# Optimization experiments

Measured on AMD Instinct MI355X. Metric: run time of the kernel, lower is better.

## Reference

```python
import jax, jax.numpy as jnp
import numpy as np

NUM_HEADS = 12

def setup_inputs() -> dict:
    key = jax.random.key(0)
    k1, k2, k3 = jax.random.split(key, 3)
    B, N, D = 16, 1024, 768
    x = jax.random.normal(k1, (B, N, D), dtype=jnp.float32)
    w_qkv = jax.random.normal(k2, (D, 3 * D), dtype=jnp.float32) * (D ** -0.5)
    b_qkv = jnp.zeros((3 * D,), dtype=jnp.float32)
    w_proj = jax.random.normal(k3, (D, D), dtype=jnp.float32) * (D ** -0.5)
    b_proj = jnp.zeros((D,), dtype=jnp.float32)
    return {"x": x, "w_qkv": w_qkv, "b_qkv": b_qkv, "w_proj": w_proj, "b_proj": b_proj}

def reference(x, w_qkv, b_qkv, w_proj, b_proj):
    B, N, D = x.shape
    H = NUM_HEADS
    Hd = D // H
    scale = Hd ** -0.5
    qkv = x @ w_qkv + b_qkv                       # (B, N, 3D)
    qkv = qkv.reshape(B, N, 3, H, Hd)
    q, k, v = qkv[:, :, 0], qkv[:, :, 1], qkv[:, :, 2]  # (B, N, H, Hd)
    attn = jnp.einsum('bnhd,bmhd->bhnm', q, k) * scale  # (B, H, N, N)
    attn = jax.nn.softmax(attn, axis=-1)
    out = jnp.einsum('bhnm,bmhd->bnhd', attn, v).reshape(B, N, D)
    return out @ w_proj + b_proj
```

## Files before the change

kernel.cpp:

```cpp
#include <hip/hip_runtime.h>


typedef _Float16 half8 __attribute__((ext_vector_type(8)));
typedef _Float16 half4 __attribute__((ext_vector_type(4)));
typedef __fp16   fp16x2 __attribute__((ext_vector_type(2)));
typedef float    f32x4  __attribute__((ext_vector_type(4)));
typedef float    f32x16 __attribute__((ext_vector_type(16)));
typedef unsigned int u32x4 __attribute__((ext_vector_type(4)));

#define DI __device__ __forceinline__

constexpr int   BATCH  = 16;
constexpr int   SEQ    = 1024;
constexpr int   DM     = 768;
constexpr int   NH     = 12;
constexpr int   HD     = 64;
constexpr float SCALE  = 0.125f;
constexpr float LOG2E  = 1.4426950408889634f;

DI void copy16(_Float16* dst, const _Float16* src) {
  *(u32x4*)dst = *(const u32x4*)src;
}

DI int pack_rtz(float a, float b) {
  union { fp16x2 h; int i; } u;
  u.h = __builtin_amdgcn_cvt_pkrtz(a, b);
  return u.i;
}

__global__ void cvt_x_kernel(const float* __restrict__ x,
                             _Float16* __restrict__ xh, int n4) {
  int i = blockIdx.x * 256 + threadIdx.x;
  if (i >= n4) return;
  float4 v = ((const float4*)x)[i];
  half4 h;
  h[0] = (_Float16)v.x; h[1] = (_Float16)v.y;
  h[2] = (_Float16)v.z; h[3] = (_Float16)v.w;
  *(half4*)(xh + (size_t)i * 4) = h;
}

__global__ void cvt_wt2_kernel(const float* __restrict__ wq,
                               _Float16* __restrict__ wqT,
                               const float* __restrict__ wp,
                               _Float16* __restrict__ wpT) {
  __shared__ float tile[32][33];
  const int by = blockIdx.y;
  const float* w; _Float16* wt; int N, nb;
  if (by < 72) { w = wq; wt = wqT; N = 2304; nb = by * 32; }
  else         { w = wp; wt = wpT; N = 768;  nb = (by - 72) * 32; }
  const int K = 768;
  int kb = blockIdx.x * 32;
  int tx = threadIdx.x & 31, ty = threadIdx.x >> 5;
#pragma unroll
  for (int i = 0; i < 32; i += 8)
    tile[ty + i][tx] = w[(size_t)(kb + ty + i) * N + nb + tx];
  __syncthreads();
#pragma unroll
  for (int i = 0; i < 32; i += 8)
    wt[(size_t)(nb + ty + i) * K + kb + tx] = (_Float16)tile[tx][ty + i];
}

__launch_bounds__(256, 3)
__global__ void gemm_qkv_kernel(const _Float16* __restrict__ A,
                                const _Float16* __restrict__ Bt,
                                const float* __restrict__ bias,
                                _Float16* __restrict__ Qo,
                                _Float16* __restrict__ Ko,
                                _Float16* __restrict__ VTo) {
  __shared__ _Float16 sh[20480];
  _Float16* Cs = sh;
  const int tid  = threadIdx.x;
  const int lin  = blockIdx.x;
  const int xcd  = lin & 7, j = lin >> 3;
  const int ct   = j % 18;
  const int m0   = ((j / 18) * 8 + xcd) * 128;
  const int n0   = ct * 128;
  const int w    = tid >> 6, lane = tid & 63;
  const int quad = lane >> 4, l15 = lane & 15;
  const int wr   = w >> 1, wc = w & 1;

  f32x4 acc[4][4] = {};

  const int e  = tid * 8;
  const int rA = e >> 5;
  const int g8 = e & 31;
  const _Float16* ga = A  + (size_t)(m0 + rA) * 768 + g8;
  const _Float16* gb = Bt + (size_t)(n0 + rA) * 768 + g8;
  const int so = rA * 40 + g8;

  u32x4 pA0 = *(const u32x4*)ga;
  u32x4 pA1 = *(const u32x4*)(ga + 64 * 768);
  u32x4 pB0 = *(const u32x4*)gb;
  u32x4 pB1 = *(const u32x4*)(gb + 64 * 768);
  {
    _Float16* As = sh; _Float16* Bs = sh + 5120;
    *(u32x4*)(As + so) = pA0; *(u32x4*)(As + so + 64 * 40) = pA1;
    *(u32x4*)(Bs + so) = pB0; *(u32x4*)(Bs + so + 64 * 40) = pB1;
  }

  for (int kt = 0; kt < 24; ++kt) {
    __syncthreads();
    if (kt < 23) {
      const int k0 = (kt + 1) * 32;
      pA0 = *(const u32x4*)(ga + k0);
      pA1 = *(const u32x4*)(ga + k0 + 64 * 768);
      pB0 = *(const u32x4*)(gb + k0);
      pB1 = *(const u32x4*)(gb + k0 + 64 * 768);
    }
    const _Float16* As = sh + (kt & 1) * 10240;
    const _Float16* Bs = As + 5120;

    half8 af[4], bf[4];
#pragma unroll
    for (int mi = 0; mi < 4; mi++)
      af[mi] = *(const half8*)&As[(wr * 64 + mi * 16 + l15) * 40 + quad * 8];
#pragma unroll
    for (int ni = 0; ni < 4; ni++)
      bf[ni] = *(const half8*)&Bs[(wc * 64 + ni * 16 + l15) * 40 + quad * 8];
#pragma unroll
    for (int mi = 0; mi < 4; mi++)
#pragma unroll
      for (int ni = 0; ni < 4; ni++)
        acc[mi][ni] = __builtin_amdgcn_mfma_f32_16x16x32_f16(
            af[mi], bf[ni], acc[mi][ni], 0, 0, 0);

    if (kt < 23) {
      _Float16* Asn = sh + ((kt + 1) & 1) * 10240;
      _Float16* Bsn = Asn + 5120;
      *(u32x4*)(Asn + so) = pA0; *(u32x4*)(Asn + so + 64 * 40) = pA1;
      *(u32x4*)(Bsn + so) = pB0; *(u32x4*)(Bsn + so + 64 * 40) = pB1;
    }
  }
  __syncthreads();

  const float oscale = (ct < 6) ? SCALE : 1.0f;
  float bcol[4];
#pragma unroll
  for (int ni = 0; ni < 4; ni++)
    bcol[ni] = bias[n0 + wc * 64 + ni * 16 + l15];

  const int b     = m0 >> 10;
  const int nrow0 = m0 & 1023;
  const int sec   = ct / 6;
  const int h0    = (ct % 6) * 2;

#pragma unroll
  for (int p = 0; p < 2; ++p) {
    if (p) __syncthreads();
    if (wr == p) {
#pragma unroll
      for (int mi = 0; mi < 4; mi++)
#pragma unroll
        for (int ni = 0; ni < 4; ni++) {
          int col = wc * 64 + ni * 16 + l15;
          int row = mi * 16 + quad * 4;
#pragma unroll
          for (int r = 0; r < 4; r++)
            Cs[(row + r) * 136 + col] =
                (_Float16)((acc[mi][ni][r] + bcol[ni]) * oscale);
        }
    }
    __syncthreads();

    if (sec < 2) {
      _Float16* dst = (sec == 0) ? Qo : Ko;
      int row = tid >> 2, seg = tid & 3;
      int hl = seg >> 1, off32 = (seg & 1) * 32;
      _Float16* g = dst +
          ((size_t)((b * NH + h0 + hl) * SEQ + nrow0 + p * 64 + row)) * HD + off32;
      const _Float16* s = &Cs[row * 136 + hl * 64 + off32];
      copy16(g, s);
      copy16(g + 8, s + 8);
      copy16(g + 16, s + 16);
      copy16(g + 24, s + 24);
    } else {
      int c = tid & 127, half = tid >> 7;
      int hl = c >> 6, d = c & 63;
      _Float16 tmp[32];
#pragma unroll
      for (int jj = 0; jj < 32; jj++) tmp[jj] = Cs[(half * 32 + jj) * 136 + c];
      _Float16* g = VTo + ((size_t)((b * NH + h0 + hl) * HD + d)) * SEQ
                        + nrow0 + p * 64 + half * 32;
#pragma unroll
      for (int jj = 0; jj < 4; jj++)
        copy16(g + jj * 8, (const _Float16*)&tmp[jj * 8]);
    }
  }
}

__launch_bounds__(256, 2)
__global__ void attn_kernel(const _Float16* __restrict__ Q,
                            const _Float16* __restrict__ K,
                            const _Float16* __restrict__ VT,
                            _Float16* __restrict__ Oh) {
  __shared__ _Float16 smem[2][2][64 * 72];
  _Float16* OLds = &smem[0][0][0];

  const int tid = threadIdx.x;
  const int i   = blockIdx.x;
  const int bh  = (i & 7) * 24 + ((i >> 3) >> 2);
  const int q0  = ((i >> 3) & 3) * 256;
  const int b   = bh / NH, hh = bh - b * NH;
  const int w   = tid >> 6, lane = tid & 63;
  const int l31 = lane & 31, h = lane >> 5;

  const _Float16* Qg = Q  + (size_t)bh * SEQ * HD;
  const _Float16* Kg = K  + (size_t)bh * SEQ * HD;
  const _Float16* Vg = VT + (size_t)bh * HD * SEQ;

  half8 qb[2][4];
#pragma unroll
  for (int N = 0; N < 2; N++) {
    const _Float16* qrow = Qg + (size_t)(q0 + w * 64 + N * 32 + l31) * HD + h * 8;
#pragma unroll
    for (int s = 0; s < 4; s++)
      qb[N][s] = *(const half8*)(qrow + s * 16);
  }

  const int  sr  = (tid & 127) >> 1;
  const int  sp  = tid & 1;
  const bool isK = tid < 128;
  const _Float16* sg = isK ? (Kg + sr * HD + sp * 32)
                           : (Vg + (size_t)sr * SEQ + sp * 32);
  const int sstep = isK ? 64 * HD : 64;
  const int soff  = (isK ? 0 : 64 * 72) + sr * 72 + sp * 32;

  u32x4 pf[4];
#pragma unroll
  for (int c = 0; c < 4; c++) pf[c] = *(const u32x4*)(sg + c * 8);
#pragma unroll
  for (int c = 0; c < 4; c++) *(u32x4*)(&smem[0][0][0] + soff + c * 8) = pf[c];

  f32x16 of[2][2];
#pragma unroll
  for (int D = 0; D < 2; D++)
#pragma unroll
    for (int N = 0; N < 2; N++)
#pragma unroll
      for (int r = 0; r < 16; r++) of[D][N][r] = 0.f;
  float m_[2] = {-1e30f, -1e30f}, l_[2] = {0.f, 0.f};

  for (int kt = 0; kt < 16; ++kt) {
    if (kt < 15) {
      const _Float16* nsg = sg + (kt + 1) * sstep;
#pragma unroll
      for (int c = 0; c < 4; c++) pf[c] = *(const u32x4*)(nsg + c * 8);
    }
    __syncthreads();
    const _Float16* Ks = &smem[kt & 1][0][0];
    const _Float16* Vs = &smem[kt & 1][1][0];

    f32x16 sf[2][2];
#pragma unroll
    for (int M = 0; M < 2; M++)
#pragma unroll
      for (int N = 0; N < 2; N++)
#pragma unroll
        for (int r = 0; r < 16; r++) sf[M][N][r] = 0.f;
#pragma unroll
    for (int s = 0; s < 4; s++) {
      half8 ka0 = *(const half8*)&Ks[l31 * 72 + s * 16 + h * 8];
      half8 ka1 = *(const half8*)&Ks[(32 + l31) * 72 + s * 16 + h * 8];
#pragma unroll
      for (int N = 0; N < 2; N++) {
        sf[0][N] = __builtin_amdgcn_mfma_f32_32x32x16_f16(ka0, qb[N][s], sf[0][N], 0, 0, 0);
        sf[1][N] = __builtin_amdgcn_mfma_f32_32x32x16_f16(ka1, qb[N][s], sf[1][N], 0, 0, 0);
      }
    }

    float alpha[2], c1[2], tsum[2];
#pragma unroll
    for (int N = 0; N < 2; N++) {
      float tmax = -1e30f;
#pragma unroll
      for (int r = 0; r < 16; r++)
        tmax = fmaxf(tmax, fmaxf(sf[0][N][r], sf[1][N][r]));
      tmax = fmaxf(tmax, __shfl_xor(tmax, 32, 64));
      float mnew = fmaxf(m_[N], tmax);
      alpha[N] = __builtin_amdgcn_exp2f((m_[N] - mnew) * LOG2E);
      m_[N] = mnew;
      c1[N] = mnew * LOG2E;
      tsum[N] = 0.f;
    }

    int pdw[2][2][8];
#pragma unroll
    for (int M = 0; M < 2; M++)
#pragma unroll
      for (int N = 0; N < 2; N++) {
#pragma unroll
        for (int r = 0; r < 16; r++) {
          float p = __builtin_amdgcn_exp2f(sf[M][N][r] * LOG2E - c1[N]);
          sf[M][N][r] = p;
          tsum[N] += p;
        }
#pragma unroll
        for (int u = 0; u < 8; u++)
          pdw[M][N][u] = pack_rtz(sf[M][N][2 * u], sf[M][N][2 * u + 1]);
      }
#pragma unroll
    for (int N = 0; N < 2; N++) {
      tsum[N] += __shfl_xor(tsum[N], 32, 64);
      l_[N] = l_[N] * alpha[N] + tsum[N];
    }
#pragma unroll
    for (int D = 0; D < 2; D++)
#pragma unroll
      for (int N = 0; N < 2; N++)
#pragma unroll
        for (int r = 0; r < 16; r++) of[D][N][r] *= alpha[N];

#pragma unroll
    for (int t = 0; t < 4; ++t) {
      const int M = t >> 1, s2 = (t & 1) * 4;
      half8 va0 = *(const half8*)&Vs[l31 * 72 + t * 16 + h * 8];
      half8 va1 = *(const half8*)&Vs[(32 + l31) * 72 + t * 16 + h * 8];
#pragma unroll
      for (int N = 0; N < 2; N++) {
        int a0 = pdw[M][N][s2 + 0], a1 = pdw[M][N][s2 + 1];
        int a2 = pdw[M][N][s2 + 2], a3 = pdw[M][N][s2 + 3];
        int e0 = h ? a0 : a2, e1 = h ? a1 : a3;
        int r0 = __shfl_xor(e0, 32, 64), r1 = __shfl_xor(e1, 32, 64);
        union { u32x4 u; half8 hv; } bb;
        bb.u[0] = h ? r0 : a0; bb.u[1] = h ? r1 : a1;
        bb.u[2] = h ? a2 : r0; bb.u[3] = h ? a3 : r1;
        of[0][N] = __builtin_amdgcn_mfma_f32_32x32x16_f16(va0, bb.hv, of[0][N], 0, 0, 0);
        of[1][N] = __builtin_amdgcn_mfma_f32_32x32x16_f16(va1, bb.hv, of[1][N], 0, 0, 0);
      }
    }

    if (kt < 15) {
      _Float16* dst = &smem[(kt + 1) & 1][0][0] + soff;
#pragma unroll
      for (int c = 0; c < 4; c++) *(u32x4*)(dst + c * 8) = pf[c];
    }
  }

  __syncthreads();
  float inv[2] = {1.0f / l_[0], 1.0f / l_[1]};
  int* OW = (int*)OLds;
#pragma unroll
  for (int N = 0; N < 2; N++) {
    const int q_local = w * 64 + N * 32 + l31;
#pragma unroll
    for (int D = 0; D < 2; D++)
#pragma unroll
      for (int u = 0; u < 8; u++) {
        int v = pack_rtz(of[D][N][2 * u] * inv[N], of[D][N][2 * u + 1] * inv[N]);
        int dwi = 16 * D + 4 * (u >> 1) + (u & 1) + 2 * h;
        OW[q_local * 36 + dwi] = v;
      }
  }
  __syncthreads();
#pragma unroll
  for (int p = 0; p < 8; p++) {
    int q = p * 32 + (tid >> 3), c = tid & 7;
    *(u32x4*)(Oh + (size_t)(b * SEQ + q0 + q) * DM + hh * HD + c * 8) =
        *(const u32x4*)&OLds[q * 72 + c * 8];
  }
}

__launch_bounds__(256, 3)
__global__ void gemm_proj_kernel(const _Float16* __restrict__ A,
                                 const _Float16* __restrict__ Bt,
                                 const float* __restrict__ bias,
                                 float* __restrict__ out) {
  __shared__ _Float16 sh[20480];
  const int tid  = threadIdx.x;
  const int lin  = blockIdx.x;
  const int xcd  = lin & 7, j = lin >> 3;
  const int ct   = j % 6;
  const int m0   = ((j / 6) * 8 + xcd) * 128;
  const int n0   = ct * 128;
  const int w    = tid >> 6, lane = tid & 63;
  const int quad = lane >> 4, l15 = lane & 15;
  const int wr   = w >> 1, wc = w & 1;

  f32x4 acc[4][4] = {};

  const int e  = tid * 8;
  const int rA = e >> 5;
  const int g8 = e & 31;
  const _Float16* ga = A  + (size_t)(m0 + rA) * 768 + g8;
  const _Float16* gb = Bt + (size_t)(n0 + rA) * 768 + g8;
  const int so = rA * 40 + g8;

  u32x4 pA0 = *(const u32x4*)ga;
  u32x4 pA1 = *(const u32x4*)(ga + 64 * 768);
  u32x4 pB0 = *(const u32x4*)gb;
  u32x4 pB1 = *(const u32x4*)(gb + 64 * 768);
  {
    _Float16* As = sh; _Float16* Bs = sh + 5120;
    *(u32x4*)(As + so) = pA0; *(u32x4*)(As + so + 64 * 40) = pA1;
    *(u32x4*)(Bs + so) = pB0; *(u32x4*)(Bs + so + 64 * 40) = pB1;
  }

  for (int kt = 0; kt < 24; ++kt) {
    __syncthreads();
    if (kt < 23) {
      const int k0 = (kt + 1) * 32;
      pA0 = *(const u32x4*)(ga + k0);
      pA1 = *(const u32x4*)(ga + k0 + 64 * 768);
      pB0 = *(const u32x4*)(gb + k0);
      pB1 = *(const u32x4*)(gb + k0 + 64 * 768);
    }
    const _Float16* As = sh + (kt & 1) * 10240;
    const _Float16* Bs = As + 5120;

    half8 af[4], bf[4];
#pragma unroll
    for (int mi = 0; mi < 4; mi++)
      af[mi] = *(const half8*)&As[(wr * 64 + mi * 16 + l15) * 40 + quad * 8];
#pragma unroll
    for (int ni = 0; ni < 4; ni++)
      bf[ni] = *(const half8*)&Bs[(wc * 64 + ni * 16 + l15) * 40 + quad * 8];
#pragma unroll
    for (int mi = 0; mi < 4; mi++)
#pragma unroll
      for (int ni = 0; ni < 4; ni++)
        acc[mi][ni] = __builtin_amdgcn_mfma_f32_16x16x32_f16(
            af[mi], bf[ni], acc[mi][ni], 0, 0, 0);

    if (kt < 23) {
      _Float16* Asn = sh + ((kt + 1) & 1) * 10240;
      _Float16* Bsn = Asn + 5120;
      *(u32x4*)(Asn + so) = pA0; *(u32x4*)(Asn + so + 64 * 40) = pA1;
      *(u32x4*)(Bsn + so) = pB0; *(u32x4*)(Bsn + so + 64 * 40) = pB1;
    }
  }

  float bcol[4];
#pragma unroll
  for (int ni = 0; ni < 4; ni++)
    bcol[ni] = bias[n0 + wc * 64 + ni * 16 + l15];
#pragma unroll
  for (int mi = 0; mi < 4; mi++)
#pragma unroll
    for (int ni = 0; ni < 4; ni++) {
      int col = n0 + wc * 64 + ni * 16 + l15;
      int row = m0 + wr * 64 + mi * 16 + quad * 4;
#pragma unroll
      for (int r = 0; r < 4; r++)
        out[(size_t)(row + r) * 768 + col] = acc[mi][ni][r] + bcol[ni];
    }
}

extern "C" void kernel_launch(void* const* d_in, const int* in_sizes, int n_in,
                              void* d_out, int out_size, void* d_ws, size_t ws_size,
                              hipStream_t stream) {
  const float* x      = (const float*)d_in[0];
  const float* w_qkv  = (const float*)d_in[1];
  const float* b_qkv  = (const float*)d_in[2];
  const float* w_proj = (const float*)d_in[3];
  const float* b_proj = (const float*)d_in[4];
  float* out = (float*)d_out;

  char* ws = (char*)d_ws;
  _Float16* xh     = (_Float16*)(ws);
  _Float16* wqkvT  = (_Float16*)(ws + 25165824);
  _Float16* wprojT = (_Float16*)(ws + 28704768);
  _Float16* Qp     = (_Float16*)(ws + 29884416);
  _Float16* Kp     = (_Float16*)(ws + 55050240);
  _Float16* VTp    = (_Float16*)(ws + 80216064);
  _Float16* Ohp    = (_Float16*)(ws + 105381888);

  cvt_x_kernel<<<dim3(3145728 / 256), 256, 0, stream>>>(x, xh, 3145728);
  cvt_wt2_kernel<<<dim3(24, 96), 256, 0, stream>>>(w_qkv, wqkvT, w_proj, wprojT);
  gemm_qkv_kernel<<<dim3(2304), 256, 0, stream>>>(xh, wqkvT, b_qkv, Qp, Kp, VTp);
  attn_kernel<<<dim3(768), 256, 0, stream>>>(Qp, Kp, VTp, Ohp);
  gemm_proj_kernel<<<dim3(768), 256, 0, stream>>>(Ohp, wprojT, b_proj, out);
}
```

Baseline: 306.5 us.

## Swizzle GEMM shared-memory tiles and raise occupancy in both projection GEMMs

Both projection GEMMs drop the padded 40-element LDS rows for dense 32-element rows with an XOR swizzle of the 16-byte slots. Write and fragment-read addresses use the same permutation, so bank conflicts stay low without padding. This shrinks LDS per block from 40 KB to 32 KB and raises the launch-bounds occupancy hint from 3 to 5 blocks per CU. The barrier now sits after the next tile's global loads are issued, letting those loads overlap it. The higher occupancy target may cap registers per thread and risks spills.

After: 725.6 us. +136.8%, slower.

```diff
diff --git a/kernel.cpp b/kernel.cpp
--- a/kernel.cpp
+++ b/kernel.cpp
@@ -60,14 +60,14 @@
     wt[(size_t)(nb + ty + i) * K + kb + tx] = (_Float16)tile[tx][ty + i];
 }
 
-__launch_bounds__(256, 3)
+__launch_bounds__(256, 5)
 __global__ void gemm_qkv_kernel(const _Float16* __restrict__ A,
                                 const _Float16* __restrict__ Bt,
                                 const float* __restrict__ bias,
                                 _Float16* __restrict__ Qo,
                                 _Float16* __restrict__ Ko,
                                 _Float16* __restrict__ VTo) {
-  __shared__ _Float16 sh[20480];
+  __shared__ _Float16 sh[16384];
   _Float16* Cs = sh;
   const int tid  = threadIdx.x;
   const int lin  = blockIdx.x;
@@ -81,25 +81,24 @@
 
   f32x4 acc[4][4] = {};
 
-  const int e  = tid * 8;
-  const int rA = e >> 5;
-  const int g8 = e & 31;
-  const _Float16* ga = A  + (size_t)(m0 + rA) * 768 + g8;
-  const _Float16* gb = Bt + (size_t)(n0 + rA) * 768 + g8;
-  const int so = rA * 40 + g8;
+  const int rA = tid >> 2;
+  const int c  = tid & 3;
+  const _Float16* ga = A  + (size_t)(m0 + rA) * 768 + c * 8;
+  const _Float16* gb = Bt + (size_t)(n0 + rA) * 768 + c * 8;
+  const int so = rA * 32 + ((c ^ ((rA ^ (rA >> 2)) & 3)) * 8);
+  const int fslot = (quad ^ ((l15 ^ (l15 >> 2)) & 3)) * 8;
 
   u32x4 pA0 = *(const u32x4*)ga;
   u32x4 pA1 = *(const u32x4*)(ga + 64 * 768);
   u32x4 pB0 = *(const u32x4*)gb;
   u32x4 pB1 = *(const u32x4*)(gb + 64 * 768);
   {
-    _Float16* As = sh; _Float16* Bs = sh + 5120;
-    *(u32x4*)(As + so) = pA0; *(u32x4*)(As + so + 64 * 40) = pA1;
-    *(u32x4*)(Bs + so) = pB0; *(u32x4*)(Bs + so + 64 * 40) = pB1;
+    _Float16* As = sh; _Float16* Bs = sh + 4096;
+    *(u32x4*)(As + so) = pA0; *(u32x4*)(As + so + 2048) = pA1;
+    *(u32x4*)(Bs + so) = pB0; *(u32x4*)(Bs + so + 2048) = pB1;
   }
 
   for (int kt = 0; kt < 24; ++kt) {
-    __syncthreads();
     if (kt < 23) {
       const int k0 = (kt + 1) * 32;
       pA0 = *(const u32x4*)(ga + k0);
@@ -107,16 +106,17 @@
       pB0 = *(const u32x4*)(gb + k0);
       pB1 = *(const u32x4*)(gb + k0 + 64 * 768);
     }
-    const _Float16* As = sh + (kt & 1) * 10240;
-    const _Float16* Bs = As + 5120;
+    __syncthreads();
+    const _Float16* As = sh + (kt & 1) * 8192;
+    const _Float16* Bs = As + 4096;
 
     half8 af[4], bf[4];
 #pragma unroll
     for (int mi = 0; mi < 4; mi++)
-      af[mi] = *(const half8*)&As[(wr * 64 + mi * 16 + l15) * 40 + quad * 8];
+      af[mi] = *(const half8*)&As[(wr * 64 + mi * 16 + l15) * 32 + fslot];
 #pragma unroll
     for (int ni = 0; ni < 4; ni++)
-      bf[ni] = *(const half8*)&Bs[(wc * 64 + ni * 16 + l15) * 40 + quad * 8];
+      bf[ni] = *(const half8*)&Bs[(wc * 64 + ni * 16 + l15) * 32 + fslot];
 #pragma unroll
     for (int mi = 0; mi < 4; mi++)
 #pragma unroll
@@ -125,10 +125,10 @@
             af[mi], bf[ni], acc[mi][ni], 0, 0, 0);
 
     if (kt < 23) {
-      _Float16* Asn = sh + ((kt + 1) & 1) * 10240;
-      _Float16* Bsn = Asn + 5120;
-      *(u32x4*)(Asn + so) = pA0; *(u32x4*)(Asn + so + 64 * 40) = pA1;
-      *(u32x4*)(Bsn + so) = pB0; *(u32x4*)(Bsn + so + 64 * 40) = pB1;
+      _Float16* Asn = sh + ((kt + 1) & 1) * 8192;
+      _Float16* Bsn = Asn + 4096;
+      *(u32x4*)(Asn + so) = pA0; *(u32x4*)(Asn + so + 2048) = pA1;
+      *(u32x4*)(Bsn + so) = pB0; *(u32x4*)(Bsn + so + 2048) = pB1;
     }
   }
   __syncthreads();
@@ -174,11 +174,11 @@
       copy16(g + 16, s + 16);
       copy16(g + 24, s + 24);
     } else {
-      int c = tid & 127, half = tid >> 7;
-      int hl = c >> 6, d = c & 63;
+      int cc = tid & 127, half = tid >> 7;
+      int hl = cc >> 6, d = cc & 63;
       _Float16 tmp[32];
 #pragma unroll
-      for (int jj = 0; jj < 32; jj++) tmp[jj] = Cs[(half * 32 + jj) * 136 + c];
+      for (int jj = 0; jj < 32; jj++) tmp[jj] = Cs[(half * 32 + jj) * 136 + cc];
       _Float16* g = VTo + ((size_t)((b * NH + h0 + hl) * HD + d)) * SEQ
                         + nrow0 + p * 64 + half * 32;
 #pragma unroll
@@ -360,12 +360,12 @@
   }
 }
 
-__launch_bounds__(256, 3)
+__launch_bounds__(256, 5)
 __global__ void gemm_proj_kernel(const _Float16* __restrict__ A,
                                  const _Float16* __restrict__ Bt,
                                  const float* __restrict__ bias,
                                  float* __restrict__ out) {
-  __shared__ _Float16 sh[20480];
+  __shared__ _Float16 sh[16384];
   const int tid  = threadIdx.x;
   const int lin  = blockIdx.x;
   const int xcd  = lin & 7, j = lin >> 3;
@@ -378,25 +378,24 @@
 
   f32x4 acc[4][4] = {};
 
-  const int e  = tid * 8;
-  const int rA = e >> 5;
-  const int g8 = e & 31;
-  const _Float16* ga = A  + (size_t)(m0 + rA) * 768 + g8;
-  const _Float16* gb = Bt + (size_t)(n0 + rA) * 768 + g8;
-  const int so = rA * 40 + g8;
+  const int rA = tid >> 2;
+  const int c  = tid & 3;
+  const _Float16* ga = A  + (size_t)(m0 + rA) * 768 + c * 8;
+  const _Float16* gb = Bt + (size_t)(n0 + rA) * 768 + c * 8;
+  const int so = rA * 32 + ((c ^ ((rA ^ (rA >> 2)) & 3)) * 8);
+  const int fslot = (quad ^ ((l15 ^ (l15 >> 2)) & 3)) * 8;
 
   u32x4 pA0 = *(const u32x4*)ga;
   u32x4 pA1 = *(const u32x4*)(ga + 64 * 768);
   u32x4 pB0 = *(const u32x4*)gb;
   u32x4 pB1 = *(const u32x4*)(gb + 64 * 768);
   {
-    _Float16* As = sh; _Float16* Bs = sh + 5120;
-    *(u32x4*)(As + so) = pA0; *(u32x4*)(As + so + 64 * 40) = pA1;
-    *(u32x4*)(Bs + so) = pB0; *(u32x4*)(Bs + so + 64 * 40) = pB1;
+    _Float16* As = sh; _Float16* Bs = sh + 4096;
+    *(u32x4*)(As + so) = pA0; *(u32x4*)(As + so + 2048) = pA1;
+    *(u32x4*)(Bs + so) = pB0; *(u32x4*)(Bs + so + 2048) = pB1;
   }
 
   for (int kt = 0; kt < 24; ++kt) {
-    __syncthreads();
     if (kt < 23) {
       const int k0 = (kt + 1) * 32;
       pA0 = *(const u32x4*)(ga + k0);
@@ -404,16 +403,17 @@
       pB0 = *(const u32x4*)(gb + k0);
       pB1 = *(const u32x4*)(gb + k0 + 64 * 768);
     }
-    const _Float16* As = sh + (kt & 1) * 10240;
-    const _Float16* Bs = As + 5120;
+    __syncthreads();
+    const _Float16* As = sh + (kt & 1) * 8192;
+    const _Float16* Bs = As + 4096;
 
     half8 af[4], bf[4];
 #pragma unroll
     for (int mi = 0; mi < 4; mi++)
-      af[mi] = *(const half8*)&As[(wr * 64 + mi * 16 + l15) * 40 + quad * 8];
+      af[mi] = *(const half8*)&As[(wr * 64 + mi * 16 + l15) * 32 + fslot];
 #pragma unroll
     for (int ni = 0; ni < 4; ni++)
-      bf[ni] = *(const half8*)&Bs[(wc * 64 + ni * 16 + l15) * 40 + quad * 8];
+      bf[ni] = *(const half8*)&Bs[(wc * 64 + ni * 16 + l15) * 32 + fslot];
 #pragma unroll
     for (int mi = 0; mi < 4; mi++)
 #pragma unroll
@@ -422,10 +422,10 @@
             af[mi], bf[ni], acc[mi][ni], 0, 0, 0);
 
     if (kt < 23) {
-      _Float16* Asn = sh + ((kt + 1) & 1) * 10240;
-      _Float16* Bsn = Asn + 5120;
-      *(u32x4*)(Asn + so) = pA0; *(u32x4*)(Asn + so + 64 * 40) = pA1;
-      *(u32x4*)(Bsn + so) = pB0; *(u32x4*)(Bsn + so + 64 * 40) = pB1;
+      _Float16* Asn = sh + ((kt + 1) & 1) * 8192;
+      _Float16* Bsn = Asn + 4096;
+      *(u32x4*)(Asn + so) = pA0; *(u32x4*)(Asn + so + 2048) = pA1;
+      *(u32x4*)(Bsn + so) = pB0; *(u32x4*)(Bsn + so + 2048) = pB1;
     }
   }
 
```
